# Kernel tuning notes

Measured on AMD Instinct MI355X. Metric: run time of the kernel, lower is better.

## Reference

```python
import jax, jax.numpy as jnp
import numpy as np

N, E, C = 4096, 32768, 64
IN, H, HEADS, L = 128, 256, 4, 2
HD = H // HEADS


def setup_inputs() -> dict:
    key = jax.random.key(0)
    ks = iter(jax.random.split(key, 40))
    s = lambda *sh: jax.random.normal(next(ks), sh, jnp.float32) * 0.05
    inp = {
        "node_features": jax.random.normal(next(ks), (N, IN), jnp.float32),
        "edges": jax.random.randint(next(ks), (E, 2), 0, N),
        "candidates": jax.random.randint(next(ks), (C, 2), 0, N),
        # GRUCell(input_dim, hidden_dim): torch layout w_ih [3H, IN], w_hh [3H, H]
        "gru_w_ih": s(3 * H, IN), "gru_w_hh": s(3 * H, H),
        "gru_b_ih": s(3 * H), "gru_b_hh": s(3 * H),
        # GraphTransformer: L layers of MHA + LN + FFN, stacked over layer dim
        "attn_in_w": s(L, 3 * H, H), "attn_in_b": s(L, 3 * H),
        "attn_out_w": s(L, H, H), "attn_out_b": s(L, H),
        "ln1_g": jnp.ones((L, H), jnp.float32), "ln1_b": jnp.zeros((L, H), jnp.float32),
        "ffn_w1": s(L, 4 * H, H), "ffn_b1": s(L, 4 * H),
        "ffn_w2": s(L, H, 4 * H), "ffn_b2": s(L, H),
        "ln2_g": jnp.ones((L, H), jnp.float32), "ln2_b": jnp.zeros((L, H), jnp.float32),
        # SCN
        "scn_w1": s(H, H), "scn_b1": s(H), "scn_w2": s(H, H), "scn_b2": s(H),
        # EdgePredictor: Linear(2H, H) -> ReLU -> Linear(H, 1)
        "ep_w1": s(H, 2 * H), "ep_b1": s(H), "ep_w2": s(1, H), "ep_b2": s(1),
    }
    return inp


def _layernorm(x, g, b, eps=1e-5):
    m = jnp.mean(x, -1, keepdims=True)
    v = jnp.mean((x - m) ** 2, -1, keepdims=True)
    return g * (x - m) / jnp.sqrt(v + eps) + b


def _mha(x, in_w, in_b, out_w, out_b):
    # x: [N, H]; torch MultiheadAttention self-attention, batch=1
    qkv = x @ in_w.T + in_b                      # [N, 3H]
    q, k, v = jnp.split(qkv, 3, axis=-1)
    q = q.reshape(N, HEADS, HD).transpose(1, 0, 2)  # [heads, N, hd]
    k = k.reshape(N, HEADS, HD).transpose(1, 0, 2)
    v = v.reshape(N, HEADS, HD).transpose(1, 0, 2)
    scores = jnp.einsum('hqd,hkd->hqk', q, k) / jnp.sqrt(jnp.float32(HD))
    a = jax.nn.softmax(scores, axis=-1)
    o = jnp.einsum('hqk,hkd->hqd', a, v).transpose(1, 0, 2).reshape(N, H)
    return o @ out_w.T + out_b


def _run_memory(node_features, edges, gru_w_ih, gru_w_hh, gru_b_ih, gru_b_hh):
    # input-gate contribution depends only on src feature: vectorize upfront
    gi_all = node_features[edges[:, 0]] @ gru_w_ih.T + gru_b_ih  # [E, 3H]

    def step(mem, inp):
        gi, dst = inp
        h = mem[dst]                                   # gather [H]
        gh = h @ gru_w_hh.T + gru_b_hh                 # [3H]
        ir, iz, inn = jnp.split(gi, 3)
        hr, hz, hn = jnp.split(gh, 3)
        r = jax.nn.sigmoid(ir + hr)
        z = jax.nn.sigmoid(iz + hz)
        n = jnp.tanh(inn + r * hn)
        h_new = (1.0 - z) * n + z * h                  # torch GRUCell update
        return mem.at[dst].set(h_new), None

    mem0 = jnp.zeros((N, H), jnp.float32)
    mem, _ = jax.lax.scan(step, mem0, (gi_all, edges[:, 1]))
    return mem


def reference(node_features, edges, candidates, gru_w_ih, gru_w_hh, gru_b_ih, gru_b_hh,
              attn_in_w, attn_in_b, attn_out_w, attn_out_b, ln1_g, ln1_b,
              ffn_w1, ffn_b1, ffn_w2, ffn_b2, ln2_g, ln2_b,
              scn_w1, scn_b1, scn_w2, scn_b2, ep_w1, ep_b1, ep_w2, ep_b2):
    mem = _run_memory(node_features, edges, gru_w_ih, gru_w_hh, gru_b_ih, gru_b_hh)
    x = jax.lax.stop_gradient(mem)   # original writes memory with .detach()
    for l in range(L):
        a = _mha(x, attn_in_w[l], attn_in_b[l], attn_out_w[l], attn_out_b[l])
        x = _layernorm(x + a, ln1_g[l], ln1_b[l])
        f = jax.nn.relu(x @ ffn_w1[l].T + ffn_b1[l]) @ ffn_w2[l].T + ffn_b2[l]
        x = _layernorm(x + f, ln2_g[l], ln2_b[l])
    refined = jax.nn.relu(x @ scn_w1.T + scn_b1) @ scn_w2.T + scn_b2
    h = jnp.concatenate([refined[candidates[:, 0]], refined[candidates[:, 1]]], axis=-1)  # [C, 2H]
    logits = jax.nn.relu(h @ ep_w1.T + ep_b1) @ ep_w2.T + ep_b2  # [C, 1]
    return jax.nn.sigmoid(logits).squeeze(-1)
```

## Files before the change

### kernel.cpp

```cpp
#include <hip/hip_runtime.h>
#include <math.h>

#define NN     4096
#define NE     32768
#define NCAND  64
#define IND    128
#define HDM    256
#define NL     2
#define MAXD   64
#define GNPB   16
#define NS     4

typedef __attribute__((ext_vector_type(8))) short short8;
typedef __attribute__((ext_vector_type(4))) short short4b;
typedef __attribute__((ext_vector_type(4))) float f32x4;

__device__ __forceinline__ float sigf(float x) { return 1.0f / (1.0f + __expf(-x)); }
__device__ __forceinline__ float tanh_fast(float x) {
  float e = __expf(-2.0f * fabsf(x));
  float r = (1.0f - e) / (1.0f + e);
  return x < 0.0f ? -r : r;
}
__device__ __forceinline__ unsigned short f2bf(float f) {
  unsigned int x = __float_as_uint(f);
  x += 0x7fffu + ((x >> 16) & 1u);
  return (unsigned short)(x >> 16);
}
__device__ __forceinline__ float bf2f(unsigned short u) {
  return __uint_as_float(((unsigned int)u) << 16);
}

#define CVT_TOT 2523136
__global__ __launch_bounds__(256) void cvt_weights(
    const float* __restrict__ nf, const float* __restrict__ wih,
    const float* __restrict__ ain, const float* __restrict__ aout,
    const float* __restrict__ f1, const float* __restrict__ f2,
    const float* __restrict__ s1, const float* __restrict__ s2,
    const float* __restrict__ whh, unsigned short* __restrict__ dst) {
  const size_t e = ((size_t)blockIdx.x * 256 + threadIdx.x) * 4;
  if (e >= CVT_TOT) return;
  const float* src;
  if (e < 524288)       src = nf   + e;
  else if (e < 622592)  src = wih  + (e - 524288);
  else if (e < 1015808) src = ain  + (e - 622592);
  else if (e < 1146880) src = aout + (e - 1015808);
  else if (e < 1671168) src = f1   + (e - 1146880);
  else if (e < 2195456) src = f2   + (e - 1671168);
  else if (e < 2260992) src = s1   + (e - 2195456);
  else if (e < 2326528) src = s2   + (e - 2260992);
  else                  src = whh  + (e - 2326528);
  const float4 v = *(const float4*)src;
  dst[e + 0] = f2bf(v.x); dst[e + 1] = f2bf(v.y);
  dst[e + 2] = f2bf(v.z); dst[e + 3] = f2bf(v.w);
}

__global__ __launch_bounds__(256) void build_pos(const int* __restrict__ edges,
                                                 int* __restrict__ cnt, int* __restrict__ lists) {
  const int e = blockIdx.x * 256 + threadIdx.x;
  const int d = edges[2 * e + 1];
  const int slot = atomicAdd(&cnt[d], 1);
  if (slot < MAXD) lists[(size_t)d * MAXD + slot] = e;
}

__global__ __launch_bounds__(256) void sort_srcs(const int* __restrict__ edges,
                                                 int* __restrict__ cnt,
                                                 const int* __restrict__ lists,
                                                 int* __restrict__ srcs,
                                                 int* __restrict__ hist) {
  __shared__ int Ls[256][65];
  const int t = threadIdx.x;
  const int d = blockIdx.x * 256 + t;
  int c = cnt[d]; if (c > MAXD) c = MAXD;
  for (int i = 0; i < c; ++i) Ls[t][i] = lists[(size_t)d * MAXD + i];
  for (int i = 1; i < c; ++i) {
    const int key = Ls[t][i];
    int j = i - 1;
    while (j >= 0 && Ls[t][j] > key) { Ls[t][j + 1] = Ls[t][j]; --j; }
    Ls[t][j + 1] = key;
  }
  for (int i = 0; i < c; ++i) srcs[(size_t)d * MAXD + i] = edges[2 * Ls[t][i]];
  cnt[d] = c;
  atomicAdd(&hist[c], 1);
}

__global__ __launch_bounds__(256) void scan_prep(const int* __restrict__ hist,
                                                 int* __restrict__ cursor,
                                                 const float* __restrict__ b_ih,
                                                 const float* __restrict__ b_hh,
                                                 float* __restrict__ bias_gx) {
  if (blockIdx.x == 3) {
    const int t = threadIdx.x;
    if (t <= MAXD) {
      int ss = 0;
      for (int dd = t + 1; dd <= MAXD; ++dd) ss += hist[dd];
      cursor[t] = ss;
    }
  } else {
    const int gt = blockIdx.x * 256 + threadIdx.x;
    if (gt < 768) bias_gx[gt] = b_ih[gt] + (gt < 512 ? b_hh[gt] : 0.0f);
  }
}

__global__ __launch_bounds__(256) void perm_scatter(const int* __restrict__ cnt,
                                                    int* __restrict__ cursor, int* __restrict__ perm) {
  const int d = blockIdx.x * 256 + threadIdx.x;
  const int rank = atomicAdd(&cursor[cnt[d]], 1);
  perm[rank] = d;
}

template <int ACT, int GS, int OMODE, int VT>
__global__ __launch_bounds__(256) void gemm_bf16(
    const unsigned short* __restrict__ A, const int* __restrict__ gidx,
    const unsigned short* __restrict__ W, const float* __restrict__ bias,
    float* __restrict__ C, unsigned short* __restrict__ Cb,
    unsigned short* __restrict__ Vt, int M, int N, int K) {
  __shared__ unsigned short As[64 * 64];
  __shared__ unsigned short Ws[64 * 64];
  __shared__ int ridx[64];
  const int bm = blockIdx.y * 64, bn = blockIdx.x * 64;
  const int tid = threadIdx.x;
  const int ln = tid & 63, w = tid >> 6;
  const int jc = ln & 15, kq = ln >> 4;
  const int srow = tid >> 2, q = tid & 3;

  if constexpr (GS > 0) {
    if (tid < 64) ridx[tid] = gidx[(size_t)(bm + tid) * GS];
    __syncthreads();
  }
  const size_t arow = (GS > 0) ? (size_t)ridx[srow] : (size_t)(bm + srow);
  const unsigned short* Asrc = A + arow * K + q * 16;
  const unsigned short* Wsrc = W + (size_t)(bn + srow) * K + q * 16;

  f32x4 acc[2][2];
#pragma unroll
  for (int i = 0; i < 2; ++i)
#pragma unroll
    for (int j = 0; j < 2; ++j) acc[i][j] = (f32x4){0.f, 0.f, 0.f, 0.f};
  const int mrow = (w >> 1) * 32, ncol = (w & 1) * 32;
  const int sb0 = (q * 32) ^ ((srow & 7) << 4);
  const int sb1 = (q * 32 + 16) ^ ((srow & 7) << 4);

  for (int k0 = 0; k0 < K; k0 += 64) {
    __syncthreads();
    {
      const short8 a0 = *(const short8*)(Asrc + k0);
      const short8 a1 = *(const short8*)(Asrc + k0 + 8);
      const short8 w0 = *(const short8*)(Wsrc + k0);
      const short8 w1 = *(const short8*)(Wsrc + k0 + 8);
      *(short8*)((char*)As + srow * 128 + sb0) = a0;
      *(short8*)((char*)As + srow * 128 + sb1) = a1;
      *(short8*)((char*)Ws + srow * 128 + sb0) = w0;
      *(short8*)((char*)Ws + srow * 128 + sb1) = w1;
    }
    __syncthreads();
#pragma unroll
    for (int kt = 0; kt < 2; ++kt) {
      const int kb = kt * 64 + kq * 16;
      short8 a[2], bb[2];
#pragma unroll
      for (int i = 0; i < 2; ++i) {
        const int ra = mrow + i * 16 + jc;
        a[i] = *(const short8*)((const char*)As + ra * 128 + (kb ^ ((ra & 7) << 4)));
        const int rb = ncol + i * 16 + jc;
        bb[i] = *(const short8*)((const char*)Ws + rb * 128 + (kb ^ ((rb & 7) << 4)));
      }
#pragma unroll
      for (int mi = 0; mi < 2; ++mi)
#pragma unroll
        for (int ni = 0; ni < 2; ++ni)
          acc[mi][ni] = __builtin_amdgcn_mfma_f32_16x16x32_bf16(a[mi], bb[ni], acc[mi][ni], 0, 0, 0);
    }
  }
#pragma unroll
  for (int mi = 0; mi < 2; ++mi)
#pragma unroll
    for (int ni = 0; ni < 2; ++ni) {
      const int col = bn + ncol + ni * 16 + jc;
      const float bs = bias[col];
      float vals[4];
#pragma unroll
      for (int v = 0; v < 4; ++v) {
        float val = acc[mi][ni][v] + bs;
        if (ACT == 1) val = fmaxf(val, 0.0f);
        vals[v] = val;
      }
#pragma unroll
      for (int v = 0; v < 4; ++v) {
        const int row = bm + mrow + mi * 16 + kq * 4 + v;
        if constexpr (OMODE != 2) C[(size_t)row * N + col] = vals[v];
        if constexpr (OMODE >= 1) Cb[(size_t)row * N + col] = f2bf(vals[v]);
      }
      if constexpr (VT == 1) {
        if (bn >= 512) {
          short4b p;
#pragma unroll
          for (int v = 0; v < 4; ++v) p[v] = (short)f2bf(vals[v]);
          *(short4b*)(Vt + (size_t)(col - 512) * NN + bm + mrow + mi * 16 + kq * 4) = p;
        }
      }
    }
}

__global__ __launch_bounds__(512) __attribute__((amdgpu_waves_per_eu(2, 2))) void gru_reg(
    const int* __restrict__ perm, const int* __restrict__ cnt,
    const int* __restrict__ srcs, const unsigned short* __restrict__ gx,
    const unsigned short* __restrict__ whhb, const float* __restrict__ b_hh,
    float* __restrict__ x, unsigned short* __restrict__ xb) {
  const int tid = threadIdx.x;
  const int w = tid >> 6;
  const int ln = tid & 63;
  const int jc = ln & 15, kq = ln >> 4;
  const int grow = tid >> 5, gpart = tid & 31;

  __shared__ unsigned short Ah[GNPB * 256];
  __shared__ unsigned short Gi[GNPB * 776];
  __shared__ int srcs_s[GNPB][MAXD];
  __shared__ int node_s[GNPB], cnt_s[GNPB];
  __shared__ int Rb_s;

  if (tid < GNPB) {
    const int node = perm[blockIdx.x * GNPB + tid];
    node_s[tid] = node;
    cnt_s[tid] = cnt[node];
  }
  for (int i = tid; i < GNPB * 256; i += 512) Ah[i] = 0;
  __syncthreads();
  for (int i = tid; i < GNPB * MAXD; i += 512)
    srcs_s[i >> 6][i & 63] = srcs[(size_t)node_s[i >> 6] * MAXD + (i & 63)];
  if (tid == 0) {
    int mx = 0;
    for (int i = 0; i < GNPB; ++i) mx = mx > cnt_s[i] ? mx : cnt_s[i];
    Rb_s = mx;
  }

  short8 W[48];
#pragma unroll
  for (int g = 0; g < 3; ++g)
#pragma unroll
    for (int ct = 0; ct < 2; ++ct) {
      const unsigned short* src =
          whhb + (size_t)(g * 256 + w * 32 + ct * 16 + jc) * 256 + kq * 8;
#pragma unroll
      for (int kt = 0; kt < 8; ++kt)
        W[(g * 2 + ct) * 8 + kt] = *(const short8*)(src + kt * 32);
    }
  float bhN[2];
  bhN[0] = b_hh[512 + w * 32 + jc];
  bhN[1] = b_hh[512 + w * 32 + 16 + jc];

  float h[8];
#pragma unroll
  for (int i = 0; i < 8; ++i) h[i] = 0.f;

  __syncthreads();
  const int Rb = Rb_s;
  const int myc = cnt_s[grow];

  short8 gv0, gv1, gv2;
  {
    const int sn = (0 < myc) ? srcs_s[grow][0] : 0;
    const unsigned short* gs = gx + (size_t)sn * 768 + gpart * 24;
    gv0 = *(const short8*)gs; gv1 = *(const short8*)(gs + 8); gv2 = *(const short8*)(gs + 16);
  }

  for (int r = 0; r < Rb; ++r) {
    {
      unsigned short* gdst = Gi + grow * 776 + gpart * 24;
      *(short8*)gdst = gv0;
      *(short8*)(gdst + 8) = gv1;
      *(short8*)(gdst + 16) = gv2;
    }
    {
      const int rn = r + 1;
      const int sn = (rn < myc) ? srcs_s[grow][rn] : 0;
      const unsigned short* gs = gx + (size_t)sn * 768 + gpart * 24;
      gv0 = *(const short8*)gs; gv1 = *(const short8*)(gs + 8); gv2 = *(const short8*)(gs + 16);
    }
    f32x4 acc[6];
#pragma unroll
    for (int i = 0; i < 6; ++i) acc[i] = (f32x4){0.f, 0.f, 0.f, 0.f};
#pragma unroll
    for (int kt = 0; kt < 8; ++kt) {
      const short8 a = *(const short8*)((const char*)Ah + jc * 512 +
                                        ((kt * 64 + kq * 16) ^ ((jc & 7) << 4)));
#pragma unroll
      for (int t = 0; t < 6; ++t)
        acc[t] = __builtin_amdgcn_mfma_f32_16x16x32_bf16(a, W[t * 8 + kt], acc[t], 0, 0, 0);
    }
    __syncthreads();
#pragma unroll
    for (int ct = 0; ct < 2; ++ct) {
      const int col = w * 32 + ct * 16 + jc;
#pragma unroll
      for (int v = 0; v < 4; ++v) {
        const int nd = kq * 4 + v;
        if (r < cnt_s[nd]) {
          const float giR = bf2f(Gi[nd * 776 + col]);
          const float giZ = bf2f(Gi[nd * 776 + 256 + col]);
          const float giN = bf2f(Gi[nd * 776 + 512 + col]);
          const float rr = sigf(giR + acc[ct][v]);
          const float zz = sigf(giZ + acc[2 + ct][v]);
          const float nn2 = tanh_fast(giN + rr * (acc[4 + ct][v] + bhN[ct]));
          const float hn = (1.0f - zz) * nn2 + zz * h[ct * 4 + v];
          h[ct * 4 + v] = hn;
          *(unsigned short*)((char*)Ah + nd * 512 + ((col * 2) ^ ((nd & 7) << 4))) = f2bf(hn);
        }
      }
    }
    __syncthreads();
  }
#pragma unroll
  for (int ct = 0; ct < 2; ++ct) {
    const int col = w * 32 + ct * 16 + jc;
#pragma unroll
    for (int v = 0; v < 4; ++v) {
      const int gnode = node_s[kq * 4 + v];
      x[(size_t)gnode * HDM + col] = h[ct * 4 + v];
      xb[(size_t)gnode * HDM + col] = f2bf(h[ct * 4 + v]);
    }
  }
}

__global__ __launch_bounds__(256) void flash_part(
    const unsigned short* __restrict__ qkvb, const unsigned short* __restrict__ vtb,
    float* __restrict__ Op, float* __restrict__ lp) {
  const int h = blockIdx.y;
  const int qb = blockIdx.x * 64;
  const int z = blockIdx.z;
  const int tid = threadIdx.x;
  const int ln = tid & 63, w = tid >> 6;
  const int jc = ln & 15, kq = ln >> 4;
  __shared__ unsigned short Ks[2][64 * 64];
  __shared__ unsigned short Vts[2][64 * 64];
  __shared__ unsigned short Ps[4][16 * 64];

  short8 aq[2];
  {
    const unsigned short* qsrc = qkvb + (size_t)(qb + w * 16 + jc) * 768 + h * 64 + kq * 8;
    aq[0] = *(const short8*)qsrc;
    aq[1] = *(const short8*)(qsrc + 32);
  }
  f32x4 accO[4];
#pragma unroll
  for (int nf = 0; nf < 4; ++nf) accO[nf] = (f32x4){0.f, 0.f, 0.f, 0.f};
  float psum[4] = {0.f, 0.f, 0.f, 0.f};

  const int srow = tid >> 2, sc = tid & 3;
  const int swb0 = (sc * 32) ^ ((srow & 7) << 4);
  const int swb1 = (sc * 32 + 16) ^ ((srow & 7) << 4);
  const int k0 = z * 1024;
  unsigned short* Pw = Ps[w];

  short8 kr0, kr1, vr0, vr1;
  {
    const unsigned short* ksrc = qkvb + (size_t)(k0 + srow) * 768 + 256 + h * 64 + sc * 16;
    kr0 = *(const short8*)ksrc; kr1 = *(const short8*)(ksrc + 8);
    const unsigned short* vsrc = vtb + (size_t)(h * 64 + srow) * 4096 + k0 + sc * 16;
    vr0 = *(const short8*)vsrc; vr1 = *(const short8*)(vsrc + 8);
  }

  for (int t = 0; t < 16; ++t) {
    const int cur = t & 1;
    *(short8*)((char*)Ks[cur] + srow * 128 + swb0) = kr0;
    *(short8*)((char*)Ks[cur] + srow * 128 + swb1) = kr1;
    *(short8*)((char*)Vts[cur] + srow * 128 + swb0) = vr0;
    *(short8*)((char*)Vts[cur] + srow * 128 + swb1) = vr1;
    {
      const int tn = t < 15 ? t + 1 : 15;
      const unsigned short* ksrc =
          qkvb + (size_t)(k0 + tn * 64 + srow) * 768 + 256 + h * 64 + sc * 16;
      kr0 = *(const short8*)ksrc; kr1 = *(const short8*)(ksrc + 8);
      const unsigned short* vsrc =
          vtb + (size_t)(h * 64 + srow) * 4096 + k0 + tn * 64 + sc * 16;
      vr0 = *(const short8*)vsrc; vr1 = *(const short8*)(vsrc + 8);
    }
    __syncthreads();
    f32x4 s[4];
#pragma unroll
    for (int kt = 0; kt < 4; ++kt) s[kt] = (f32x4){0.f, 0.f, 0.f, 0.f};
    __builtin_amdgcn_s_setprio(1);
#pragma unroll
    for (int ks = 0; ks < 2; ++ks) {
#pragma unroll
      for (int kt = 0; kt < 4; ++kt) {
        const int brow = kt * 16 + jc;
        const short8 bk = *(const short8*)((const char*)Ks[cur] + brow * 128 +
                                           ((ks * 64 + kq * 16) ^ ((brow & 7) << 4)));
        s[kt] = __builtin_amdgcn_mfma_f32_16x16x32_bf16(aq[ks], bk, s[kt], 0, 0, 0);
      }
    }
    __builtin_amdgcn_s_setprio(0);
#pragma unroll
    for (int kt = 0; kt < 4; ++kt) {
#pragma unroll
      for (int v = 0; v < 4; ++v) {
        const float pv = __expf(s[kt][v] * 0.125f - 8.0f);
        psum[v] += pv;
        const int pr = kq * 4 + v;
        const int cb = kt * 32 + jc * 2;
        *(unsigned short*)((char*)Pw + pr * 128 + (cb ^ ((pr & 7) << 4))) = f2bf(pv);
      }
    }
    asm volatile("s_waitcnt lgkmcnt(0)" ::: "memory");
    __builtin_amdgcn_sched_barrier(0);
    __builtin_amdgcn_s_setprio(1);
#pragma unroll
    for (int ks = 0; ks < 2; ++ks) {
      const short8 ap = *(const short8*)((const char*)Pw + jc * 128 +
                                         ((ks * 64 + kq * 16) ^ ((jc & 7) << 4)));
#pragma unroll
      for (int nf = 0; nf < 4; ++nf) {
        const int brow = nf * 16 + jc;
        const short8 bv = *(const short8*)((const char*)Vts[cur] + brow * 128 +
                                           ((ks * 64 + kq * 16) ^ ((brow & 7) << 4)));
        accO[nf] = __builtin_amdgcn_mfma_f32_16x16x32_bf16(ap, bv, accO[nf], 0, 0, 0);
      }
    }
    __builtin_amdgcn_s_setprio(0);
  }
#pragma unroll
  for (int v = 0; v < 4; ++v) {
    float ps = psum[v];
    ps += __shfl_xor(ps, 1);
    ps += __shfl_xor(ps, 2);
    ps += __shfl_xor(ps, 4);
    ps += __shfl_xor(ps, 8);
    psum[v] = ps;
  }
  float* opb = Op + ((size_t)z * NN + qb + w * 16 + kq * 4) * HDM + h * 64 + jc;
#pragma unroll
  for (int nf = 0; nf < 4; ++nf)
#pragma unroll
    for (int v = 0; v < 4; ++v)
      opb[(size_t)v * HDM + nf * 16] = accO[nf][v];
  if (jc == 0) {
#pragma unroll
    for (int v = 0; v < 4; ++v)
      lp[((size_t)z * 4 + h) * NN + qb + w * 16 + kq * 4 + v] = psum[v];
  }
}

__global__ __launch_bounds__(256) void attn_combine(const float* __restrict__ Op,
                                                    const float* __restrict__ lp,
                                                    unsigned short* __restrict__ outb) {
  const int row = blockIdx.x * 4 + (threadIdx.x >> 6);
  const int lane = threadIdx.x & 63;
  const int col = lane * 4;
  const int h = col >> 6;
  float l = 0.f;
  float4 o = {0.f, 0.f, 0.f, 0.f};
#pragma unroll
  for (int z = 0; z < NS; ++z) {
    l += lp[((size_t)z * 4 + h) * NN + row];
    const float4 p = *(const float4*)(Op + ((size_t)z * NN + row) * HDM + col);
    o.x += p.x; o.y += p.y; o.z += p.z; o.w += p.w;
  }
  const float inv = 1.0f / l;
  unsigned short* d = outb + (size_t)row * HDM + col;
  d[0] = f2bf(o.x * inv); d[1] = f2bf(o.y * inv);
  d[2] = f2bf(o.z * inv); d[3] = f2bf(o.w * inv);
}

__global__ __launch_bounds__(256) void ln_residual(float* __restrict__ x,
                                                   const float* __restrict__ a,
                                                   const float* __restrict__ g,
                                                   const float* __restrict__ b,
                                                   unsigned short* __restrict__ xb) {
  const int lane = threadIdx.x & 63;
  const int row = blockIdx.x * 4 + (threadIdx.x >> 6);
  float v[4];
  float s = 0.0f;
#pragma unroll
  for (int j = 0; j < 4; j++) {
    const int col = j * 64 + lane;
    v[j] = x[(size_t)row * HDM + col] + a[(size_t)row * HDM + col];
    s += v[j];
  }
#pragma unroll
  for (int off = 32; off > 0; off >>= 1) s += __shfl_xor(s, off);
  const float mu = s * (1.0f / HDM);
  float vs = 0.0f;
#pragma unroll
  for (int j = 0; j < 4; j++) {
    const float d = v[j] - mu;
    vs += d * d;
  }
#pragma unroll
  for (int off = 32; off > 0; off >>= 1) vs += __shfl_xor(vs, off);
  const float rinv = 1.0f / sqrtf(vs * (1.0f / HDM) + 1e-5f);
#pragma unroll
  for (int j = 0; j < 4; j++) {
    const int col = j * 64 + lane;
    const float val = g[col] * (v[j] - mu) * rinv + b[col];
    x[(size_t)row * HDM + col] = val;
    xb[(size_t)row * HDM + col] = f2bf(val);
  }
}

__global__ __launch_bounds__(256) void ep_fused(const float* __restrict__ refined,
                                                const int* __restrict__ cand,
                                                const float* __restrict__ e1w,
                                                const float* __restrict__ e1b,
                                                const float* __restrict__ e2w,
                                                const float* __restrict__ e2b,
                                                float* __restrict__ out) {
  const int c = blockIdx.x;
  const int t = threadIdx.x;
  __shared__ float hrow[512];
  __shared__ float eph_s[256];
  const int n0 = cand[2 * c], n1 = cand[2 * c + 1];
  hrow[t] = refined[(size_t)n0 * HDM + t];
  hrow[256 + t] = refined[(size_t)n1 * HDM + t];
  __syncthreads();
  const float4* wrow = (const float4*)(e1w + (size_t)t * 512);
  float s = 0.f;
#pragma unroll 8
  for (int k = 0; k < 128; ++k) {
    const float4 w4 = wrow[k];
    const float4 h4 = *(const float4*)(hrow + k * 4);
    s += w4.x * h4.x + w4.y * h4.y + w4.z * h4.z + w4.w * h4.w;
  }
  eph_s[t] = fmaxf(s + e1b[t], 0.0f);
  __syncthreads();
  if (t < 64) {
    float p = 0.f;
#pragma unroll
    for (int j = 0; j < 4; ++j) p += eph_s[j * 64 + t] * e2w[j * 64 + t];
#pragma unroll
    for (int off = 32; off > 0; off >>= 1) p += __shfl_xor(p, off);
    if (t == 0) out[c] = 1.0f / (1.0f + __expf(-(p + e2b[0])));
  }
}

extern "C" void kernel_launch(void* const* d_in, const int* in_sizes, int n_in,
                              void* d_out, int out_size, void* d_ws, size_t ws_size,
                              hipStream_t stream) {
  (void)in_sizes; (void)n_in; (void)out_size; (void)ws_size;
  const float* nf    = (const float*)d_in[0];
  const int*   edges = (const int*)d_in[1];
  const int*   cand  = (const int*)d_in[2];
  const float* w_ih  = (const float*)d_in[3];
  const float* w_hh  = (const float*)d_in[4];
  const float* b_ih  = (const float*)d_in[5];
  const float* b_hh  = (const float*)d_in[6];
  const float* ain_w = (const float*)d_in[7];
  const float* ain_b = (const float*)d_in[8];
  const float* aout_w = (const float*)d_in[9];
  const float* aout_b = (const float*)d_in[10];
  const float* ln1g = (const float*)d_in[11];
  const float* ln1b = (const float*)d_in[12];
  const float* f1w  = (const float*)d_in[13];
  const float* f1b  = (const float*)d_in[14];
  const float* f2w  = (const float*)d_in[15];
  const float* f2b  = (const float*)d_in[16];
  const float* ln2g = (const float*)d_in[17];
  const float* ln2b = (const float*)d_in[18];
  const float* s1w  = (const float*)d_in[19];
  const float* s1b  = (const float*)d_in[20];
  const float* s2w  = (const float*)d_in[21];
  const float* s2b  = (const float*)d_in[22];
  const float* e1w  = (const float*)d_in[23];
  const float* e1b  = (const float*)d_in[24];
  const float* e2w  = (const float*)d_in[25];
  const float* e2b  = (const float*)d_in[26];
  float* out = (float*)d_out;

  char* wp = (char*)d_ws;
  float* x        = (float*)wp; wp += (size_t)NN * HDM * 4;
  unsigned short* xb = (unsigned short*)wp; wp += (size_t)NN * HDM * 2;
  unsigned short* wseg = (unsigned short*)wp; wp += (size_t)CVT_TOT * 2;
  int* cnt        = (int*)wp;  wp += (size_t)NN * 4;
  int* lists      = (int*)wp;  wp += (size_t)NN * MAXD * 4;
  int* srcs       = (int*)wp;  wp += (size_t)NN * MAXD * 4;
  int* meta       = (int*)wp;  wp += 256 * 4;
  float* bias_gx  = (float*)wp; wp += 1024 * 4;
  int* perm       = (int*)wp;  wp += (size_t)NN * 4;
  unsigned short* gx = (unsigned short*)wp; wp += (size_t)NN * 768 * 2;
  char* uni       = wp;
  unsigned short* qkvb   = (unsigned short*)uni;
  unsigned short* vtb    = (unsigned short*)(uni + 6291456);
  float* abuf    = (float*)(uni + 8388608);
  unsigned short* abuf_b = (unsigned short*)(uni + 12582912);
  float* fbuf    = (float*)(uni + 14680064);
  float* Op      = fbuf;
  unsigned short* fbuf_b = (unsigned short*)(uni + 31457280);
  float* lp      = (float*)(uni + 31457280);
  float* refined = (float*)(uni + 39845888);

  unsigned short* nf_b  = wseg;
  unsigned short* wihb  = wseg + 524288;
  unsigned short* ainb  = wseg + 622592;
  unsigned short* aoutb = wseg + 1015808;
  unsigned short* f1b_  = wseg + 1146880;
  unsigned short* f2b_  = wseg + 1671168;
  unsigned short* s1b_  = wseg + 2195456;
  unsigned short* s2b_  = wseg + 2260992;
  unsigned short* whhb  = wseg + 2326528;

  int* hist   = meta;
  int* cursor = meta + 128;

  hipMemsetAsync(cnt, 0, (size_t)NN * 4, stream);
  hipMemsetAsync(meta, 0, 256 * 4, stream);

  cvt_weights<<<2464, 256, 0, stream>>>(nf, w_ih, ain_w, aout_w, f1w, f2w, s1w, s2w, w_hh, wseg);
  build_pos<<<NE / 256, 256, 0, stream>>>(edges, cnt, lists);
  sort_srcs<<<NN / 256, 256, 0, stream>>>(edges, cnt, lists, srcs, hist);
  scan_prep<<<4, 256, 0, stream>>>(hist, cursor, b_ih, b_hh, bias_gx);
  perm_scatter<<<NN / 256, 256, 0, stream>>>(cnt, cursor, perm);

  gemm_bf16<0, 0, 2, 0><<<dim3(12, NN / 64), 256, 0, stream>>>(
      nf_b, nullptr, wihb, bias_gx, nullptr, gx, nullptr, NN, 768, IND);
  gru_reg<<<NN / GNPB, 512, 0, stream>>>(perm, cnt, srcs, gx, whhb, b_hh, x, xb);

  for (int l = 0; l < NL; l++) {
    gemm_bf16<0, 0, 2, 1><<<dim3(12, 64), 256, 0, stream>>>(
        xb, nullptr, ainb + (size_t)l * 196608, ain_b + l * 768, nullptr, qkvb, vtb, NN, 768, HDM);
    flash_part<<<dim3(64, 4, NS), 256, 0, stream>>>(qkvb, vtb, Op, lp);
    attn_combine<<<NN / 4, 256, 0, stream>>>(Op, lp, abuf_b);
    gemm_bf16<0, 0, 0, 0><<<dim3(4, 64), 256, 0, stream>>>(
        abuf_b, nullptr, aoutb + (size_t)l * 65536, aout_b + l * 256, fbuf, nullptr, nullptr, NN, 256, HDM);
    ln_residual<<<NN / 4, 256, 0, stream>>>(x, fbuf, ln1g + l * 256, ln1b + l * 256, xb);
    gemm_bf16<1, 0, 2, 0><<<dim3(16, 64), 256, 0, stream>>>(
        xb, nullptr, f1b_ + (size_t)l * 262144, f1b + l * 1024, nullptr, fbuf_b, nullptr, NN, 1024, HDM);
    gemm_bf16<0, 0, 0, 0><<<dim3(4, 64), 256, 0, stream>>>(
        fbuf_b, nullptr, f2b_ + (size_t)l * 262144, f2b + l * 256, abuf, nullptr, nullptr, NN, 256, 1024);
    ln_residual<<<NN / 4, 256, 0, stream>>>(x, abuf, ln2g + l * 256, ln2b + l * 256, xb);
  }

  gemm_bf16<1, 0, 2, 0><<<dim3(4, 64), 256, 0, stream>>>(
      xb, nullptr, s1b_, s1b, nullptr, abuf_b, nullptr, NN, 256, HDM);
  gemm_bf16<0, 0, 0, 0><<<dim3(4, 64), 256, 0, stream>>>(
      abuf_b, nullptr, s2b_, s2b, refined, nullptr, nullptr, NN, 256, HDM);
  ep_fused<<<NCAND, 256, 0, stream>>>(refined, cand, e1w, e1b, e2w, e2b, out);
}
```

Before: 355.9 us.

## Double GRU block to 16 waves, one column tile per wave, drop gx prefetch

The GRU recurrence kernel now runs 1024 threads per block. Each wave owns a single 16-column tile across the three gates, so the per-thread register-resident W_hh fragment drops from 48 to 24 short8 values, and waves_per_eu rises from 2 to 4. Each wave also gathers its own node's gx row directly in the current step, replacing the cross-row software prefetch of the next step. The aim is more latency hiding through more resident waves per step, at the cost of losing the one-step-ahead gx prefetch and adding more barrier participants.

```diff
diff --git a/kernel.cpp b/kernel.cpp
--- a/kernel.cpp
+++ b/kernel.cpp
@@ -201,7 +201,7 @@
     }
 }
 
-__global__ __launch_bounds__(512) __attribute__((amdgpu_waves_per_eu(2, 2))) void gru_reg(
+__global__ __launch_bounds__(1024) __attribute__((amdgpu_waves_per_eu(4, 4))) void gru_reg(
     const int* __restrict__ perm, const int* __restrict__ cnt,
     const int* __restrict__ srcs, const unsigned short* __restrict__ gx,
     const unsigned short* __restrict__ whhb, const float* __restrict__ b_hh,
@@ -210,7 +210,7 @@
   const int w = tid >> 6;
   const int ln = tid & 63;
   const int jc = ln & 15, kq = ln >> 4;
-  const int grow = tid >> 5, gpart = tid & 31;
+  const int gpart = ln;
 
   __shared__ unsigned short Ah[GNPB * 256];
   __shared__ unsigned short Gi[GNPB * 776];
@@ -223,101 +223,84 @@
     node_s[tid] = node;
     cnt_s[tid] = cnt[node];
   }
-  for (int i = tid; i < GNPB * 256; i += 512) Ah[i] = 0;
+  for (int i = tid; i < GNPB * 256; i += 1024) Ah[i] = 0;
   __syncthreads();
-  for (int i = tid; i < GNPB * MAXD; i += 512)
+  {
+    const int i = tid;
     srcs_s[i >> 6][i & 63] = srcs[(size_t)node_s[i >> 6] * MAXD + (i & 63)];
+  }
   if (tid == 0) {
     int mx = 0;
     for (int i = 0; i < GNPB; ++i) mx = mx > cnt_s[i] ? mx : cnt_s[i];
     Rb_s = mx;
   }
 
-  short8 W[48];
-#pragma unroll
-  for (int g = 0; g < 3; ++g)
-#pragma unroll
-    for (int ct = 0; ct < 2; ++ct) {
-      const unsigned short* src =
-          whhb + (size_t)(g * 256 + w * 32 + ct * 16 + jc) * 256 + kq * 8;
-#pragma unroll
-      for (int kt = 0; kt < 8; ++kt)
-        W[(g * 2 + ct) * 8 + kt] = *(const short8*)(src + kt * 32);
-    }
-  float bhN[2];
-  bhN[0] = b_hh[512 + w * 32 + jc];
-  bhN[1] = b_hh[512 + w * 32 + 16 + jc];
-
-  float h[8];
-#pragma unroll
-  for (int i = 0; i < 8; ++i) h[i] = 0.f;
+  short8 W[24];
+#pragma unroll
+  for (int g = 0; g < 3; ++g) {
+    const unsigned short* src =
+        whhb + (size_t)(g * 256 + w * 16 + jc) * 256 + kq * 8;
+#pragma unroll
+    for (int kt = 0; kt < 8; ++kt)
+      W[g * 8 + kt] = *(const short8*)(src + kt * 32);
+  }
+  const int col = w * 16 + jc;
+  const float bhN = b_hh[512 + col];
+
+  float h[4];
+#pragma unroll
+  for (int i = 0; i < 4; ++i) h[i] = 0.f;
 
   __syncthreads();
   const int Rb = Rb_s;
-  const int myc = cnt_s[grow];
-
-  short8 gv0, gv1, gv2;
-  {
-    const int sn = (0 < myc) ? srcs_s[grow][0] : 0;
-    const unsigned short* gs = gx + (size_t)sn * 768 + gpart * 24;
-    gv0 = *(const short8*)gs; gv1 = *(const short8*)(gs + 8); gv2 = *(const short8*)(gs + 16);
-  }
+  const int myc = cnt_s[w];
 
   for (int r = 0; r < Rb; ++r) {
-    {
-      unsigned short* gdst = Gi + grow * 776 + gpart * 24;
-      *(short8*)gdst = gv0;
-      *(short8*)(gdst + 8) = gv1;
-      *(short8*)(gdst + 16) = gv2;
-    }
-    {
-      const int rn = r + 1;
-      const int sn = (rn < myc) ? srcs_s[grow][rn] : 0;
-      const unsigned short* gs = gx + (size_t)sn * 768 + gpart * 24;
-      gv0 = *(const short8*)gs; gv1 = *(const short8*)(gs + 8); gv2 = *(const short8*)(gs + 16);
-    }
-    f32x4 acc[6];
-#pragma unroll
-    for (int i = 0; i < 6; ++i) acc[i] = (f32x4){0.f, 0.f, 0.f, 0.f};
+    const int sn = (r < myc) ? srcs_s[w][r] : 0;
+    const unsigned short* gs = gx + (size_t)sn * 768;
+    const short8 ga = *(const short8*)(gs + gpart * 8);
+    short8 gb_;
+    const int idx1 = 64 + gpart;
+    if (idx1 < 96) gb_ = *(const short8*)(gs + idx1 * 8);
+    f32x4 acc[3];
+#pragma unroll
+    for (int i = 0; i < 3; ++i) acc[i] = (f32x4){0.f, 0.f, 0.f, 0.f};
 #pragma unroll
     for (int kt = 0; kt < 8; ++kt) {
       const short8 a = *(const short8*)((const char*)Ah + jc * 512 +
                                         ((kt * 64 + kq * 16) ^ ((jc & 7) << 4)));
 #pragma unroll
-      for (int t = 0; t < 6; ++t)
-        acc[t] = __builtin_amdgcn_mfma_f32_16x16x32_bf16(a, W[t * 8 + kt], acc[t], 0, 0, 0);
+      for (int g = 0; g < 3; ++g)
+        acc[g] = __builtin_amdgcn_mfma_f32_16x16x32_bf16(a, W[g * 8 + kt], acc[g], 0, 0, 0);
+    }
+    {
+      unsigned short* gdst = Gi + w * 776;
+      *(short8*)(gdst + gpart * 8) = ga;
+      if (idx1 < 96) *(short8*)(gdst + idx1 * 8) = gb_;
     }
     __syncthreads();
 #pragma unroll
-    for (int ct = 0; ct < 2; ++ct) {
-      const int col = w * 32 + ct * 16 + jc;
-#pragma unroll
-      for (int v = 0; v < 4; ++v) {
-        const int nd = kq * 4 + v;
-        if (r < cnt_s[nd]) {
-          const float giR = bf2f(Gi[nd * 776 + col]);
-          const float giZ = bf2f(Gi[nd * 776 + 256 + col]);
-          const float giN = bf2f(Gi[nd * 776 + 512 + col]);
-          const float rr = sigf(giR + acc[ct][v]);
-          const float zz = sigf(giZ + acc[2 + ct][v]);
-          const float nn2 = tanh_fast(giN + rr * (acc[4 + ct][v] + bhN[ct]));
-          const float hn = (1.0f - zz) * nn2 + zz * h[ct * 4 + v];
-          h[ct * 4 + v] = hn;
-          *(unsigned short*)((char*)Ah + nd * 512 + ((col * 2) ^ ((nd & 7) << 4))) = f2bf(hn);
-        }
+    for (int v = 0; v < 4; ++v) {
+      const int nd = kq * 4 + v;
+      if (r < cnt_s[nd]) {
+        const float giR = bf2f(Gi[nd * 776 + col]);
+        const float giZ = bf2f(Gi[nd * 776 + 256 + col]);
+        const float giN = bf2f(Gi[nd * 776 + 512 + col]);
+        const float rr = sigf(giR + acc[0][v]);
+        const float zz = sigf(giZ + acc[1][v]);
+        const float nn2 = tanh_fast(giN + rr * (acc[2][v] + bhN));
+        const float hn = (1.0f - zz) * nn2 + zz * h[v];
+        h[v] = hn;
+        *(unsigned short*)((char*)Ah + nd * 512 + ((col * 2) ^ ((nd & 7) << 4))) = f2bf(hn);
       }
     }
     __syncthreads();
   }
 #pragma unroll
-  for (int ct = 0; ct < 2; ++ct) {
-    const int col = w * 32 + ct * 16 + jc;
-#pragma unroll
-    for (int v = 0; v < 4; ++v) {
-      const int gnode = node_s[kq * 4 + v];
-      x[(size_t)gnode * HDM + col] = h[ct * 4 + v];
-      xb[(size_t)gnode * HDM + col] = f2bf(h[ct * 4 + v]);
-    }
+  for (int v = 0; v < 4; ++v) {
+    const int gnode = node_s[kq * 4 + v];
+    x[(size_t)gnode * HDM + col] = h[v];
+    xb[(size_t)gnode * HDM + col] = f2bf(h[v]);
   }
 }
 
@@ -611,7 +594,7 @@
 
   gemm_bf16<0, 0, 2, 0><<<dim3(12, NN / 64), 256, 0, stream>>>(
       nf_b, nullptr, wihb, bias_gx, nullptr, gx, nullptr, NN, 768, IND);
-  gru_reg<<<NN / GNPB, 512, 0, stream>>>(perm, cnt, srcs, gx, whhb, b_hh, x, xb);
+  gru_reg<<<NN / GNPB, 1024, 0, stream>>>(perm, cnt, srcs, gx, whhb, b_hh, x, xb);
 
   for (int l = 0; l < NL; l++) {
     gemm_bf16<0, 0, 2, 1><<<dim3(12, 64), 256, 0, stream>>>(
```

Measured after the change: 386.2 us. 1.09x slower.

## Stream z/n GRU weights from memory, drop prefetch, fold memsets into conversion kernel

Applied to the files above, without the earlier changes.

In the GRU kernel, only the reset-gate hidden weights stay in registers. The update and new-gate weights are now re-read from global memory (L1/L2) on every recurrence step, and the waves-per-EU attribute is removed. This cuts register pressure so more waves can be resident, at the cost of extra per-step weight loads. The one-step-ahead register prefetch of gate inputs becomes a same-iteration load whose LDS store is placed after the MFMAs. The two memsets that cleared the count and meta buffers are folded into the weight-conversion kernel to save launches.

```diff
diff --git a/kernel.cpp b/kernel.cpp
--- a/kernel.cpp
+++ b/kernel.cpp
@@ -36,7 +36,10 @@
     const float* __restrict__ ain, const float* __restrict__ aout,
     const float* __restrict__ f1, const float* __restrict__ f2,
     const float* __restrict__ s1, const float* __restrict__ s2,
-    const float* __restrict__ whh, unsigned short* __restrict__ dst) {
+    const float* __restrict__ whh, unsigned short* __restrict__ dst,
+    int* __restrict__ cnt, int* __restrict__ meta) {
+  if (blockIdx.x < 16) cnt[blockIdx.x * 256 + threadIdx.x] = 0;
+  else if (blockIdx.x == 16) meta[threadIdx.x] = 0;
   const size_t e = ((size_t)blockIdx.x * 256 + threadIdx.x) * 4;
   if (e >= CVT_TOT) return;
   const float* src;
@@ -201,7 +204,7 @@
     }
 }
 
-__global__ __launch_bounds__(512) __attribute__((amdgpu_waves_per_eu(2, 2))) void gru_reg(
+__global__ __launch_bounds__(512) void gru_reg(
     const int* __restrict__ perm, const int* __restrict__ cnt,
     const int* __restrict__ srcs, const unsigned short* __restrict__ gx,
     const unsigned short* __restrict__ whhb, const float* __restrict__ b_hh,
@@ -233,17 +236,19 @@
     Rb_s = mx;
   }
 
-  short8 W[48];
-#pragma unroll
-  for (int g = 0; g < 3; ++g)
-#pragma unroll
-    for (int ct = 0; ct < 2; ++ct) {
-      const unsigned short* src =
-          whhb + (size_t)(g * 256 + w * 32 + ct * 16 + jc) * 256 + kq * 8;
-#pragma unroll
-      for (int kt = 0; kt < 8; ++kt)
-        W[(g * 2 + ct) * 8 + kt] = *(const short8*)(src + kt * 32);
-    }
+  short8 Wr[16];
+#pragma unroll
+  for (int ct = 0; ct < 2; ++ct) {
+    const unsigned short* src = whhb + (size_t)(w * 32 + ct * 16 + jc) * 256 + kq * 8;
+#pragma unroll
+    for (int kt = 0; kt < 8; ++kt)
+      Wr[ct * 8 + kt] = *(const short8*)(src + kt * 32);
+  }
+  const short8* pz0 = (const short8*)(whhb + (size_t)(256 + w * 32 + jc) * 256 + kq * 8);
+  const short8* pz1 = (const short8*)(whhb + (size_t)(256 + w * 32 + 16 + jc) * 256 + kq * 8);
+  const short8* pn0 = (const short8*)(whhb + (size_t)(512 + w * 32 + jc) * 256 + kq * 8);
+  const short8* pn1 = (const short8*)(whhb + (size_t)(512 + w * 32 + 16 + jc) * 256 + kq * 8);
+
   float bhN[2];
   bhN[0] = b_hh[512 + w * 32 + jc];
   bhN[1] = b_hh[512 + w * 32 + 16 + jc];
@@ -256,26 +261,13 @@
   const int Rb = Rb_s;
   const int myc = cnt_s[grow];
 
-  short8 gv0, gv1, gv2;
-  {
-    const int sn = (0 < myc) ? srcs_s[grow][0] : 0;
+  for (int r = 0; r < Rb; ++r) {
+    asm volatile("" ::: "memory");
+    const int sn = (r < myc) ? srcs_s[grow][r] : 0;
     const unsigned short* gs = gx + (size_t)sn * 768 + gpart * 24;
-    gv0 = *(const short8*)gs; gv1 = *(const short8*)(gs + 8); gv2 = *(const short8*)(gs + 16);
-  }
-
-  for (int r = 0; r < Rb; ++r) {
-    {
-      unsigned short* gdst = Gi + grow * 776 + gpart * 24;
-      *(short8*)gdst = gv0;
-      *(short8*)(gdst + 8) = gv1;
-      *(short8*)(gdst + 16) = gv2;
-    }
-    {
-      const int rn = r + 1;
-      const int sn = (rn < myc) ? srcs_s[grow][rn] : 0;
-      const unsigned short* gs = gx + (size_t)sn * 768 + gpart * 24;
-      gv0 = *(const short8*)gs; gv1 = *(const short8*)(gs + 8); gv2 = *(const short8*)(gs + 16);
-    }
+    const short8 g0 = *(const short8*)gs;
+    const short8 g1 = *(const short8*)(gs + 8);
+    const short8 g2 = *(const short8*)(gs + 16);
     f32x4 acc[6];
 #pragma unroll
     for (int i = 0; i < 6; ++i) acc[i] = (f32x4){0.f, 0.f, 0.f, 0.f};
@@ -283,9 +275,22 @@
     for (int kt = 0; kt < 8; ++kt) {
       const short8 a = *(const short8*)((const char*)Ah + jc * 512 +
                                         ((kt * 64 + kq * 16) ^ ((jc & 7) << 4)));
-#pragma unroll
-      for (int t = 0; t < 6; ++t)
-        acc[t] = __builtin_amdgcn_mfma_f32_16x16x32_bf16(a, W[t * 8 + kt], acc[t], 0, 0, 0);
+      acc[0] = __builtin_amdgcn_mfma_f32_16x16x32_bf16(a, Wr[kt], acc[0], 0, 0, 0);
+      acc[1] = __builtin_amdgcn_mfma_f32_16x16x32_bf16(a, Wr[8 + kt], acc[1], 0, 0, 0);
+      const short8 wz0 = pz0[kt * 4];
+      const short8 wz1 = pz1[kt * 4];
+      const short8 wn0 = pn0[kt * 4];
+      const short8 wn1 = pn1[kt * 4];
+      acc[2] = __builtin_amdgcn_mfma_f32_16x16x32_bf16(a, wz0, acc[2], 0, 0, 0);
+      acc[3] = __builtin_amdgcn_mfma_f32_16x16x32_bf16(a, wz1, acc[3], 0, 0, 0);
+      acc[4] = __builtin_amdgcn_mfma_f32_16x16x32_bf16(a, wn0, acc[4], 0, 0, 0);
+      acc[5] = __builtin_amdgcn_mfma_f32_16x16x32_bf16(a, wn1, acc[5], 0, 0, 0);
+    }
+    {
+      unsigned short* gd = Gi + grow * 776 + gpart * 24;
+      *(short8*)gd = g0;
+      *(short8*)(gd + 8) = g1;
+      *(short8*)(gd + 16) = g2;
     }
     __syncthreads();
 #pragma unroll
@@ -600,10 +605,8 @@
   int* hist   = meta;
   int* cursor = meta + 128;
 
-  hipMemsetAsync(cnt, 0, (size_t)NN * 4, stream);
-  hipMemsetAsync(meta, 0, 256 * 4, stream);
-
-  cvt_weights<<<2464, 256, 0, stream>>>(nf, w_ih, ain_w, aout_w, f1w, f2w, s1w, s2w, w_hh, wseg);
+  cvt_weights<<<2464, 256, 0, stream>>>(nf, w_ih, ain_w, aout_w, f1w, f2w, s1w, s2w, w_hh,
+                                        wseg, cnt, meta);
   build_pos<<<NE / 256, 256, 0, stream>>>(edges, cnt, lists);
   sort_srcs<<<NN / 256, 256, 0, stream>>>(edges, cnt, lists, srcs, hist);
   scan_prep<<<4, 256, 0, stream>>>(hist, cursor, b_ih, b_hh, bias_gx);
```

New measurement: 438.8 us. 1.23x slower.
